# Kernel optimization log

Measured on AMD Instinct MI355X. Metric: run time of the kernel, lower is better.

The kernel has to match this reference:

```python
import jax, jax.numpy as jnp
import numpy as np

HEADS = 8
NQ = 4  # n_qubits


def _apply_rx(state, q, theta):
    # state: (M,2,2,2,2) complex, theta: (M,)
    c = jnp.cos(theta / 2).astype(jnp.complex64)
    s = (-1j * jnp.sin(theta / 2)).astype(jnp.complex64)
    g = jnp.stack([jnp.stack([c, s], -1), jnp.stack([s, c], -1)], -2)  # (M,2,2)
    st = jnp.moveaxis(state, 1 + q, 1)
    st = jnp.einsum('mab,mb...->ma...', g, st)
    return jnp.moveaxis(st, 1, 1 + q)


def _apply_cnot(state, c, t):
    st = jnp.moveaxis(state, [1 + c, 1 + t], [1, 2])  # (M,2(ctrl),2(tgt),...)
    st = jnp.concatenate([st[:, :1], st[:, 1:, ::-1]], axis=1)
    return jnp.moveaxis(st, [1, 2], [1 + c, 1 + t])


def vqc(x, weights):
    # x: (M,4) embedding angles; weights: (L,4) layer RX angles
    M = x.shape[0]
    state = jnp.zeros((M, 2, 2, 2, 2), jnp.complex64).at[:, 0, 0, 0, 0].set(1.0)
    for q in range(NQ):  # AngleEmbedding (RX)
        state = _apply_rx(state, q, x[:, q])
    for l in range(weights.shape[0]):  # BasicEntanglerLayers
        for q in range(NQ):
            state = _apply_rx(state, q, jnp.broadcast_to(weights[l, q], (M,)))
        for q in range(NQ):
            state = _apply_cnot(state, q, (q + 1) % NQ)
    probs = state.real ** 2 + state.imag ** 2  # (M,2,2,2,2)
    z = [jnp.moveaxis(probs, 1 + q, 1)[:, 0].sum((1, 2, 3))
         - jnp.moveaxis(probs, 1 + q, 1)[:, 1].sum((1, 2, 3)) for q in range(NQ)]
    return jnp.stack(z, -1)  # (M,4) PauliZ expvals


def setup_inputs() -> dict:
    key = jax.random.key(0)
    ks = jax.random.split(key, 24)
    B, S, E = 16, 512, 512
    D = E // HEADS
    f = jax.random.normal
    inp = {
        'query': f(ks[0], (B, S, E), jnp.float32),
        'key': f(ks[1], (B, S, E), jnp.float32),
        'value': f(ks[2], (B, S, E), jnp.float32),
        'mask': jnp.ones((B, S, S), jnp.int32),
        'Wq_in': f(ks[3], (NQ, D), jnp.float32) / np.sqrt(D),
        'bq_in': f(ks[4], (NQ,), jnp.float32) / np.sqrt(D),
        'Wk_in': f(ks[5], (NQ, D), jnp.float32) / np.sqrt(D),
        'bk_in': f(ks[6], (NQ,), jnp.float32) / np.sqrt(D),
        'Wv_in': f(ks[7], (NQ, D), jnp.float32) / np.sqrt(D),
        'bv_in': f(ks[8], (NQ,), jnp.float32) / np.sqrt(D),
        'wvq': f(ks[9], (1, NQ), jnp.float32),
        'wvk': f(ks[10], (1, NQ), jnp.float32),
        'wvv': f(ks[11], (1, NQ), jnp.float32),
        'Wq': f(ks[12], (D, NQ), jnp.float32) / np.sqrt(NQ),
        'bq': f(ks[13], (D,), jnp.float32) / np.sqrt(NQ),
        'Wk': f(ks[14], (D, NQ), jnp.float32) / np.sqrt(NQ),
        'bk': f(ks[15], (D,), jnp.float32) / np.sqrt(NQ),
        'Wv': f(ks[16], (D, NQ), jnp.float32) / np.sqrt(NQ),
        'bv': f(ks[17], (D,), jnp.float32) / np.sqrt(NQ),
        'Wo': f(ks[18], (E, 2 * E), jnp.float32) / np.sqrt(2 * E),
        'bo': f(ks[19], (E,), jnp.float32) / np.sqrt(2 * E),
    }
    return inp


def reference(query, key, value, mask, Wq_in, bq_in, Wk_in, bk_in, Wv_in, bv_in,
              wvq, wvk, wvv, Wq, bq, Wk, bk, Wv, bv, Wo, bo):
    B, S, E = query.shape
    H = HEADS
    D = E // H

    def project(x, W_in, b_in, w_vqc, W_out, b_out):
        xh = x.reshape(B, S, H, D)
        xin = jnp.einsum('bshd,qd->bshq', xh, W_in) + b_in  # (B,S,H,NQ)
        xq = vqc(xin.reshape(-1, NQ), w_vqc).reshape(B, S, H, NQ)
        return jnp.einsum('bshq,dq->bshd', xq, W_out) + b_out  # (B,S,H,D)

    Q = project(query, Wq_in, bq_in, wvq, Wq, bq)
    K = project(key, Wk_in, bk_in, wvk, Wk, bk)
    V = project(value, Wv_in, bv_in, wvv, Wv, bv)

    energy = jnp.einsum('bqhd,bkhd->bhqk', Q, K)
    # NOTE: original masked_fill result is discarded (no-op); scale is depth/2
    # due to Python precedence (depth**1/2 == depth/2). Reproduced faithfully.
    attn = jax.nn.softmax(energy / (D / 2.0), axis=-1)
    out = jnp.einsum('bhqv,bvhd->bqhd', attn, V).reshape(B, S, H * D)
    Qf = Q.reshape(B, S, H * D)
    cat = jnp.concatenate([Qf, out], axis=-1)  # (B,S,2E)
    return cat @ Wo.T + bo
```

## Files before the change

kernel.cpp:

```cpp
#include <hip/hip_runtime.h>
#include <hip/hip_bf16.h>

#define B_ 16
#define S_ 512
#define E_ 512
#define H_ 8
#define D_ 64

typedef __hip_bfloat16 bf16;
typedef unsigned short u16;
typedef __attribute__((ext_vector_type(8))) short short8;
typedef __attribute__((ext_vector_type(4))) float floatx4;

__device__ __forceinline__ u16 f2b(float x) {
    bf16 h = __float2bfloat16(x);
    return *reinterpret_cast<u16*>(&h);
}
__device__ __forceinline__ short8 ld8(const u16* p) { return *(const short8*)p; }

template<int CTRL>
__device__ __forceinline__ float qperm(float x) {
    return __builtin_bit_cast(float,
        __builtin_amdgcn_update_dpp(0, __builtin_bit_cast(int, x), CTRL, 0xF, 0xF, true));
}

#define PROJ_ROW_BLOCKS 3072

__global__ __launch_bounds__(256) void proj_kernel(
    const float* __restrict__ q_in, const float* __restrict__ k_in, const float* __restrict__ v_in,
    const float* __restrict__ Wq_in, const float* __restrict__ bq_in,
    const float* __restrict__ Wk_in, const float* __restrict__ bk_in,
    const float* __restrict__ Wv_in, const float* __restrict__ bv_in,
    const float* __restrict__ wvq, const float* __restrict__ wvk, const float* __restrict__ wvv,
    const float* __restrict__ Wq, const float* __restrict__ bq,
    const float* __restrict__ Wk, const float* __restrict__ bk,
    const float* __restrict__ Wv, const float* __restrict__ bv,
    const float* __restrict__ Wo, u16* __restrict__ Wb,
    u16* __restrict__ Qb, u16* __restrict__ Kb, u16* __restrict__ Vb)
{
    if (blockIdx.x >= PROJ_ROW_BLOCKS) {
        const int i = ((blockIdx.x - PROJ_ROW_BLOCKS) * 256 + threadIdx.x) * 8;
        const float4 a = *(const float4*)&Wo[i];
        const float4 b4 = *(const float4*)&Wo[i + 4];
        u16 tmp[8] __attribute__((aligned(16)));
        tmp[0] = f2b(a.x); tmp[1] = f2b(a.y); tmp[2] = f2b(a.z); tmp[3] = f2b(a.w);
        tmp[4] = f2b(b4.x); tmp[5] = f2b(b4.y); tmp[6] = f2b(b4.z); tmp[7] = f2b(b4.w);
        *(short8*)&Wb[i] = *(short8*)tmp;
        return;
    }

    __shared__ __align__(16) float sWin[256];
    __shared__ __align__(16) float sWout[256];
    __shared__ __align__(16) float sbout[64];
    __shared__ float4 sbw;

    const int t = threadIdx.x;
    const int p = blockIdx.x >> 10;

    const float *X, *Win, *bin, *wv, *Wout, *bout;
    u16* dst;
    if (p == 0)      { X = q_in; Win = Wq_in; bin = bq_in; wv = wvq; Wout = Wq; bout = bq; dst = Qb; }
    else if (p == 1) { X = k_in; Win = Wk_in; bin = bk_in; wv = wvk; Wout = Wk; bout = bk; dst = Kb; }
    else             { X = v_in; Win = Wv_in; bin = bv_in; wv = wvv; Wout = Wv; bout = bv; dst = Vb; }

    sWin[t] = Win[t];
    sWout[t] = Wout[t];
    if (t < 64) sbout[t] = bout[t];
    if (t == 0) sbw = make_float4(bin[0] + wv[0], bin[1] + wv[1],
                                  bin[2] + wv[2], bin[3] + wv[3]);
    __syncthreads();

    const int j = t & 3;
    const int m = (blockIdx.x & 1023) * 64 + (t >> 2);
    const int d0 = j * 16;

    const float* xp = X + (size_t)m * 64 + d0;
    float4 xv[4];
#pragma unroll
    for (int i = 0; i < 4; ++i) xv[i] = *(const float4*)(xp + i * 4);

    float part[4] = {0.f, 0.f, 0.f, 0.f};
#pragma unroll
    for (int i = 0; i < 4; ++i) {
#pragma unroll
        for (int q = 0; q < 4; ++q) {
            const float4 w4 = *(const float4*)&sWin[q * 64 + d0 + i * 4];
            part[q] = fmaf(xv[i].x, w4.x, fmaf(xv[i].y, w4.y,
                      fmaf(xv[i].z, w4.z, fmaf(xv[i].w, w4.w, part[q]))));
        }
    }
#pragma unroll
    for (int q = 0; q < 4; ++q) {
        part[q] += qperm<0xB1>(part[q]);
        part[q] += qperm<0x4E>(part[q]);
    }

    const float4 bw = sbw;
    const float c0 = __cosf(part[0] + bw.x);
    const float c1 = __cosf(part[1] + bw.y);
    const float c2 = __cosf(part[2] + bw.z);
    const float c3 = __cosf(part[3] + bw.w);
    const float tt = c2 * c3;
    const float z1 = c0 * c1;
    const float z0 = c1 * tt;
    const float z2 = z1 * c2;
    const float z3 = z1 * tt;

    const int b = m >> 12, s = (m >> 3) & 511, h = m & 7;
    u16* op = dst + ((size_t)(b * 4096 + h * 512 + s)) * 64 + d0;

    u16 tmp[16] __attribute__((aligned(16)));
#pragma unroll
    for (int d = 0; d < 16; ++d) {
        const float4 wo = *(const float4*)&sWout[(d0 + d) * 4];
        const float o = fmaf(z0, wo.x, fmaf(z1, wo.y,
                        fmaf(z2, wo.z, fmaf(z3, wo.w, sbout[d0 + d]))));
        tmp[d] = f2b(o);
    }
    *(short8*)op = *(short8*)tmp;
    *(short8*)(op + 8) = *(short8*)(tmp + 8);
}

__global__ __launch_bounds__(256) void attn_kernel(
    const u16* __restrict__ Qb, const u16* __restrict__ Kb, const u16* __restrict__ Vb,
    u16* __restrict__ Ob)
{
    __shared__ __align__(16) u16 Ks[64][72];
    __shared__ __align__(16) u16 Vt[64][72];
    __shared__ __align__(16) u16 Ps[4][32][72];

    const int t = threadIdx.x, lane = t & 63, w = t >> 6;
    const int bh = blockIdx.x >> 2;
    const int q0 = (blockIdx.x & 3) * 128;
    const int b = bh >> 3, h = bh & 7;

    const u16* Qp = Qb + (size_t)bh * (S_ * D_) + (size_t)q0 * D_;
    const u16* Kp = Kb + (size_t)bh * (S_ * D_);
    const u16* Vp = Vb + (size_t)bh * (S_ * D_);

    const int nl = lane & 15;
    const int kg = (lane >> 4) * 8;

    short8 qa[2][2];
#pragma unroll
    for (int mt = 0; mt < 2; ++mt) {
        qa[mt][0] = ld8(&Qp[(w * 32 + mt * 16 + nl) * 64 + kg]);
        qa[mt][1] = ld8(&Qp[(w * 32 + mt * 16 + nl) * 64 + kg + 32]);
    }

    floatx4 of[2][4];
    float l_run[2][4];
#pragma unroll
    for (int mt = 0; mt < 2; ++mt)
#pragma unroll
        for (int r = 0; r < 4; ++r) { l_run[mt][r] = 0.f; }
#pragma unroll
    for (int mt = 0; mt < 2; ++mt)
#pragma unroll
        for (int nt = 0; nt < 4; ++nt) of[mt][nt] = 0.f;

    const int rK = t & 63, cK = (t >> 6) * 8;
    const int vr0 = (t & 31) * 2, vc = (t >> 5) * 8;

    short8 kA = ld8(&Kp[rK * 64 + cK]);
    short8 kB = ld8(&Kp[rK * 64 + cK + 32]);
    short8 vA = ld8(&Vp[vr0 * 64 + vc]);
    short8 vB = ld8(&Vp[(vr0 + 1) * 64 + vc]);

    for (int ch = 0; ch < 8; ++ch) {
        __syncthreads();
        *(short8*)&Ks[rK][cK] = kA;
        *(short8*)&Ks[rK][cK + 32] = kB;
#pragma unroll
        for (int jj = 0; jj < 8; ++jj) {
            const unsigned pack = (u16)((short*)&vA)[jj] |
                                  ((unsigned)(u16)((short*)&vB)[jj] << 16);
            *(unsigned*)&Vt[vc + jj][vr0] = pack;
        }
        if (ch < 7) {
            const int nb = (ch + 1) * 64;
            kA = ld8(&Kp[(nb + rK) * 64 + cK]);
            kB = ld8(&Kp[(nb + rK) * 64 + cK + 32]);
            vA = ld8(&Vp[(nb + vr0) * 64 + vc]);
            vB = ld8(&Vp[(nb + vr0 + 1) * 64 + vc]);
        }
        __syncthreads();

        floatx4 sf[2][4];
#pragma unroll
        for (int mt = 0; mt < 2; ++mt)
#pragma unroll
            for (int nt = 0; nt < 4; ++nt) sf[mt][nt] = 0.f;
#pragma unroll
        for (int nt = 0; nt < 4; ++nt) {
            const short8 kf0 = ld8(&Ks[nt * 16 + nl][kg]);
            const short8 kf1 = ld8(&Ks[nt * 16 + nl][kg + 32]);
#pragma unroll
            for (int mt = 0; mt < 2; ++mt) {
                sf[mt][nt] = __builtin_amdgcn_mfma_f32_16x16x32_bf16(qa[mt][0], kf0, sf[mt][nt], 0, 0, 0);
                sf[mt][nt] = __builtin_amdgcn_mfma_f32_16x16x32_bf16(qa[mt][1], kf1, sf[mt][nt], 0, 0, 0);
            }
        }

        const int prow = (lane >> 4) * 4;
#pragma unroll
        for (int mt = 0; mt < 2; ++mt)
#pragma unroll
            for (int nt = 0; nt < 4; ++nt) {
#pragma unroll
                for (int r = 0; r < 4; ++r) {
                    const float pv = __expf(sf[mt][nt][r] * 0.03125f);
                    l_run[mt][r] += pv;
                    Ps[w][mt * 16 + prow + r][nt * 16 + nl] = f2b(pv);
                }
            }

        short8 pa[2][2];
#pragma unroll
        for (int mt = 0; mt < 2; ++mt) {
            pa[mt][0] = ld8(&Ps[w][mt * 16 + nl][kg]);
            pa[mt][1] = ld8(&Ps[w][mt * 16 + nl][kg + 32]);
        }
#pragma unroll
        for (int nt = 0; nt < 4; ++nt) {
            const short8 vf0 = ld8(&Vt[nt * 16 + nl][kg]);
            const short8 vf1 = ld8(&Vt[nt * 16 + nl][kg + 32]);
#pragma unroll
            for (int mt = 0; mt < 2; ++mt) {
                of[mt][nt] = __builtin_amdgcn_mfma_f32_16x16x32_bf16(pa[mt][0], vf0, of[mt][nt], 0, 0, 0);
                of[mt][nt] = __builtin_amdgcn_mfma_f32_16x16x32_bf16(pa[mt][1], vf1, of[mt][nt], 0, 0, 0);
            }
        }
    }

#pragma unroll
    for (int mt = 0; mt < 2; ++mt) {
        float inv[4];
#pragma unroll
        for (int r = 0; r < 4; ++r) {
            float sum = l_run[mt][r];
#pragma unroll
            for (int off = 1; off < 16; off <<= 1) sum += __shfl_xor(sum, off, 64);
            inv[r] = 1.0f / sum;
        }
        const int srow = q0 + w * 32 + mt * 16 + (lane >> 4) * 4;
#pragma unroll
        for (int r = 0; r < 4; ++r) {
            const size_t base = ((size_t)(b * S_ + srow + r)) * E_ + h * 64 + nl;
#pragma unroll
            for (int nt = 0; nt < 4; ++nt)
                Ob[base + nt * 16] = f2b(of[mt][nt][r] * inv[r]);
        }
    }
}

__global__ __launch_bounds__(256) void out_kernel(
    const u16* __restrict__ Qb, const u16* __restrict__ Ob,
    const u16* __restrict__ Wb, const float* __restrict__ bo,
    float* __restrict__ out)
{
    __shared__ __align__(16) u16 As[64][72];
    __shared__ __align__(16) u16 Bs[128][72];

    const int t = threadIdx.x, lane = t & 63, w = t >> 6;
    const int e0 = (blockIdx.x & 3) * 128;
    const int n0 = (blockIdx.x >> 2) * 64;
    const int wr = (w >> 1) * 32, wc = (w & 1) * 64;
    const int nl = lane & 15, kg = (lane >> 4) * 8;

    const int rA = t & 63, cA = (t >> 6) * 8;
    const int rB = t & 127, cB0 = (t >> 7) * 8;
    const u16* wrow = &Wb[(size_t)(e0 + rB) * 1024];

    floatx4 acc[2][4];
#pragma unroll
    for (int i = 0; i < 2; ++i)
#pragma unroll
        for (int jq = 0; jq < 4; ++jq) acc[i][jq] = 0.f;

    auto a_src = [&](int j0, int r, int c) -> const u16* {
        const int n = n0 + r;
        return (j0 < 512)
            ? &Qb[(((size_t)(n >> 9) * 8 + (j0 >> 6)) * 512 + (n & 511)) * 64 + c]
            : &Ob[(size_t)n * 512 + (j0 - 512) + c];
    };

    short8 aA = ld8(a_src(0, rA, cA));
    short8 aB = ld8(a_src(0, rA, cA + 32));
    short8 b0 = ld8(wrow + cB0);
    short8 b1 = ld8(wrow + cB0 + 16);
    short8 b2 = ld8(wrow + cB0 + 32);
    short8 b3 = ld8(wrow + cB0 + 48);

    for (int j0 = 0; j0 < 1024; j0 += 64) {
        __syncthreads();
        *(short8*)&As[rA][cA] = aA;
        *(short8*)&As[rA][cA + 32] = aB;
        *(short8*)&Bs[rB][cB0] = b0;
        *(short8*)&Bs[rB][cB0 + 16] = b1;
        *(short8*)&Bs[rB][cB0 + 32] = b2;
        *(short8*)&Bs[rB][cB0 + 48] = b3;
        if (j0 < 960) {
            const int jn = j0 + 64;
            aA = ld8(a_src(jn, rA, cA));
            aB = ld8(a_src(jn, rA, cA + 32));
            b0 = ld8(wrow + jn + cB0);
            b1 = ld8(wrow + jn + cB0 + 16);
            b2 = ld8(wrow + jn + cB0 + 32);
            b3 = ld8(wrow + jn + cB0 + 48);
        }
        __syncthreads();

        short8 af[2][2], bfr[4][2];
#pragma unroll
        for (int mt = 0; mt < 2; ++mt) {
            af[mt][0] = ld8(&As[wr + mt * 16 + nl][kg]);
            af[mt][1] = ld8(&As[wr + mt * 16 + nl][kg + 32]);
        }
#pragma unroll
        for (int nt = 0; nt < 4; ++nt) {
            bfr[nt][0] = ld8(&Bs[wc + nt * 16 + nl][kg]);
            bfr[nt][1] = ld8(&Bs[wc + nt * 16 + nl][kg + 32]);
        }
#pragma unroll
        for (int mt = 0; mt < 2; ++mt)
#pragma unroll
            for (int nt = 0; nt < 4; ++nt) {
                acc[mt][nt] = __builtin_amdgcn_mfma_f32_16x16x32_bf16(af[mt][0], bfr[nt][0], acc[mt][nt], 0, 0, 0);
                acc[mt][nt] = __builtin_amdgcn_mfma_f32_16x16x32_bf16(af[mt][1], bfr[nt][1], acc[mt][nt], 0, 0, 0);
            }
    }

    const int prow = (lane >> 4) * 4;
#pragma unroll
    for (int mt = 0; mt < 2; ++mt)
#pragma unroll
        for (int r = 0; r < 4; ++r) {
            const int n = n0 + wr + mt * 16 + prow + r;
#pragma unroll
            for (int nt = 0; nt < 4; ++nt) {
                const int e = e0 + wc + nt * 16 + nl;
                out[(size_t)n * 512 + e] = acc[mt][nt][r] + bo[e];
            }
        }
}

extern "C" void kernel_launch(void* const* d_in, const int* in_sizes, int n_in,
                              void* d_out, int out_size, void* d_ws, size_t ws_size,
                              hipStream_t stream)
{
    const float* q_in  = (const float*)d_in[0];
    const float* k_in  = (const float*)d_in[1];
    const float* v_in  = (const float*)d_in[2];
    const float* Wq_in = (const float*)d_in[4];
    const float* bq_in = (const float*)d_in[5];
    const float* Wk_in = (const float*)d_in[6];
    const float* bk_in = (const float*)d_in[7];
    const float* Wv_in = (const float*)d_in[8];
    const float* bv_in = (const float*)d_in[9];
    const float* wvq   = (const float*)d_in[10];
    const float* wvk   = (const float*)d_in[11];
    const float* wvv   = (const float*)d_in[12];
    const float* Wq    = (const float*)d_in[13];
    const float* bq    = (const float*)d_in[14];
    const float* Wk    = (const float*)d_in[15];
    const float* bk    = (const float*)d_in[16];
    const float* Wv    = (const float*)d_in[17];
    const float* bv    = (const float*)d_in[18];
    const float* Wo    = (const float*)d_in[19];
    const float* bo    = (const float*)d_in[20];

    u16* ws = (u16*)d_ws;
    u16* Qb = ws;
    u16* Kb = ws + (size_t)(1 << 22);
    u16* Vb = ws + (size_t)(2 << 22);
    u16* Ob = ws + (size_t)3 * (1 << 22);
    u16* Wb = ws + (size_t)4 * (1 << 22);

    proj_kernel<<<PROJ_ROW_BLOCKS + 256, 256, 0, stream>>>(q_in, k_in, v_in,
        Wq_in, bq_in, Wk_in, bk_in, Wv_in, bv_in,
        wvq, wvk, wvv, Wq, bq, Wk, bk, Wv, bv,
        Wo, Wb, Qb, Kb, Vb);
    attn_kernel<<<512, 256, 0, stream>>>(Qb, Kb, Vb, Ob);
    out_kernel<<<512, 256, 0, stream>>>(Qb, Ob, Wb, bo, (float*)d_out);
}
```

Baseline: 186.0 us.

## Load MFMA operand fragments directly from global memory, dropping LDS staging for K and GEMM

```diff
diff --git a/kernel.cpp b/kernel.cpp
--- a/kernel.cpp
+++ b/kernel.cpp
@@ -121,11 +121,10 @@
     *(short8*)(op + 8) = *(short8*)(tmp + 8);
 }
 
-__global__ __launch_bounds__(256) void attn_kernel(
+__global__ __launch_bounds__(256, 2) void attn_kernel(
     const u16* __restrict__ Qb, const u16* __restrict__ Kb, const u16* __restrict__ Vb,
     u16* __restrict__ Ob)
 {
-    __shared__ __align__(16) u16 Ks[64][72];
     __shared__ __align__(16) u16 Vt[64][72];
     __shared__ __align__(16) u16 Ps[4][32][72];
 
@@ -153,24 +152,26 @@
 #pragma unroll
     for (int mt = 0; mt < 2; ++mt)
 #pragma unroll
-        for (int r = 0; r < 4; ++r) { l_run[mt][r] = 0.f; }
+        for (int r = 0; r < 4; ++r) l_run[mt][r] = 0.f;
 #pragma unroll
     for (int mt = 0; mt < 2; ++mt)
 #pragma unroll
         for (int nt = 0; nt < 4; ++nt) of[mt][nt] = 0.f;
 
-    const int rK = t & 63, cK = (t >> 6) * 8;
     const int vr0 = (t & 31) * 2, vc = (t >> 5) * 8;
 
-    short8 kA = ld8(&Kp[rK * 64 + cK]);
-    short8 kB = ld8(&Kp[rK * 64 + cK + 32]);
+    short8 kf[2][4][2];
+#pragma unroll
+    for (int nt = 0; nt < 4; ++nt) {
+        kf[0][nt][0] = ld8(&Kp[(nt * 16 + nl) * 64 + kg]);
+        kf[0][nt][1] = ld8(&Kp[(nt * 16 + nl) * 64 + kg + 32]);
+    }
     short8 vA = ld8(&Vp[vr0 * 64 + vc]);
     short8 vB = ld8(&Vp[(vr0 + 1) * 64 + vc]);
 
     for (int ch = 0; ch < 8; ++ch) {
+        const int cur = ch & 1, nxt = cur ^ 1;
         __syncthreads();
-        *(short8*)&Ks[rK][cK] = kA;
-        *(short8*)&Ks[rK][cK + 32] = kB;
 #pragma unroll
         for (int jj = 0; jj < 8; ++jj) {
             const unsigned pack = (u16)((short*)&vA)[jj] |
@@ -179,8 +180,11 @@
         }
         if (ch < 7) {
             const int nb = (ch + 1) * 64;
-            kA = ld8(&Kp[(nb + rK) * 64 + cK]);
-            kB = ld8(&Kp[(nb + rK) * 64 + cK + 32]);
+#pragma unroll
+            for (int nt = 0; nt < 4; ++nt) {
+                kf[nxt][nt][0] = ld8(&Kp[(nb + nt * 16 + nl) * 64 + kg]);
+                kf[nxt][nt][1] = ld8(&Kp[(nb + nt * 16 + nl) * 64 + kg + 32]);
+            }
             vA = ld8(&Vp[(nb + vr0) * 64 + vc]);
             vB = ld8(&Vp[(nb + vr0 + 1) * 64 + vc]);
         }
@@ -193,12 +197,10 @@
             for (int nt = 0; nt < 4; ++nt) sf[mt][nt] = 0.f;
 #pragma unroll
         for (int nt = 0; nt < 4; ++nt) {
-            const short8 kf0 = ld8(&Ks[nt * 16 + nl][kg]);
-            const short8 kf1 = ld8(&Ks[nt * 16 + nl][kg + 32]);
 #pragma unroll
             for (int mt = 0; mt < 2; ++mt) {
-                sf[mt][nt] = __builtin_amdgcn_mfma_f32_16x16x32_bf16(qa[mt][0], kf0, sf[mt][nt], 0, 0, 0);
-                sf[mt][nt] = __builtin_amdgcn_mfma_f32_16x16x32_bf16(qa[mt][1], kf1, sf[mt][nt], 0, 0, 0);
+                sf[mt][nt] = __builtin_amdgcn_mfma_f32_16x16x32_bf16(qa[mt][0], kf[cur][nt][0], sf[mt][nt], 0, 0, 0);
+                sf[mt][nt] = __builtin_amdgcn_mfma_f32_16x16x32_bf16(qa[mt][1], kf[cur][nt][1], sf[mt][nt], 0, 0, 0);
             }
         }
 
@@ -254,80 +256,69 @@
     }
 }
 
-__global__ __launch_bounds__(256) void out_kernel(
+__global__ __launch_bounds__(256, 2) void out_kernel(
     const u16* __restrict__ Qb, const u16* __restrict__ Ob,
     const u16* __restrict__ Wb, const float* __restrict__ bo,
     float* __restrict__ out)
 {
-    __shared__ __align__(16) u16 As[64][72];
-    __shared__ __align__(16) u16 Bs[128][72];
-
-    const int t = threadIdx.x, lane = t & 63, w = t >> 6;
+    const int lane = threadIdx.x & 63, w = threadIdx.x >> 6;
     const int e0 = (blockIdx.x & 3) * 128;
     const int n0 = (blockIdx.x >> 2) * 64;
     const int wr = (w >> 1) * 32, wc = (w & 1) * 64;
     const int nl = lane & 15, kg = (lane >> 4) * 8;
 
-    const int rA = t & 63, cA = (t >> 6) * 8;
-    const int rB = t & 127, cB0 = (t >> 7) * 8;
-    const u16* wrow = &Wb[(size_t)(e0 + rB) * 1024];
-
     floatx4 acc[2][4];
 #pragma unroll
     for (int i = 0; i < 2; ++i)
 #pragma unroll
         for (int jq = 0; jq < 4; ++jq) acc[i][jq] = 0.f;
 
-    auto a_src = [&](int j0, int r, int c) -> const u16* {
-        const int n = n0 + r;
+    const int an[2] = { n0 + wr + nl, n0 + wr + 16 + nl };
+    const u16* wrow[4];
+#pragma unroll
+    for (int nt = 0; nt < 4; ++nt)
+        wrow[nt] = &Wb[(size_t)(e0 + wc + nt * 16 + nl) * 1024];
+
+    auto a_src = [&](int j0, int n, int c) -> const u16* {
         return (j0 < 512)
             ? &Qb[(((size_t)(n >> 9) * 8 + (j0 >> 6)) * 512 + (n & 511)) * 64 + c]
             : &Ob[(size_t)n * 512 + (j0 - 512) + c];
     };
 
-    short8 aA = ld8(a_src(0, rA, cA));
-    short8 aB = ld8(a_src(0, rA, cA + 32));
-    short8 b0 = ld8(wrow + cB0);
-    short8 b1 = ld8(wrow + cB0 + 16);
-    short8 b2 = ld8(wrow + cB0 + 32);
-    short8 b3 = ld8(wrow + cB0 + 48);
-
-    for (int j0 = 0; j0 < 1024; j0 += 64) {
-        __syncthreads();
-        *(short8*)&As[rA][cA] = aA;
-        *(short8*)&As[rA][cA + 32] = aB;
-        *(short8*)&Bs[rB][cB0] = b0;
-        *(short8*)&Bs[rB][cB0 + 16] = b1;
-        *(short8*)&Bs[rB][cB0 + 32] = b2;
-        *(short8*)&Bs[rB][cB0 + 48] = b3;
-        if (j0 < 960) {
-            const int jn = j0 + 64;
-            aA = ld8(a_src(jn, rA, cA));
-            aB = ld8(a_src(jn, rA, cA + 32));
-            b0 = ld8(wrow + jn + cB0);
-            b1 = ld8(wrow + jn + cB0 + 16);
-            b2 = ld8(wrow + jn + cB0 + 32);
-            b3 = ld8(wrow + jn + cB0 + 48);
-        }
-        __syncthreads();
-
-        short8 af[2][2], bfr[4][2];
-#pragma unroll
-        for (int mt = 0; mt < 2; ++mt) {
-            af[mt][0] = ld8(&As[wr + mt * 16 + nl][kg]);
-            af[mt][1] = ld8(&As[wr + mt * 16 + nl][kg + 32]);
-        }
-#pragma unroll
-        for (int nt = 0; nt < 4; ++nt) {
-            bfr[nt][0] = ld8(&Bs[wc + nt * 16 + nl][kg]);
-            bfr[nt][1] = ld8(&Bs[wc + nt * 16 + nl][kg + 32]);
+    short8 af[2][2][2], bf[2][4][2];
+#pragma unroll
+    for (int mt = 0; mt < 2; ++mt) {
+        af[0][mt][0] = ld8(a_src(0, an[mt], kg));
+        af[0][mt][1] = ld8(a_src(0, an[mt], kg + 32));
+    }
+#pragma unroll
+    for (int nt = 0; nt < 4; ++nt) {
+        bf[0][nt][0] = ld8(wrow[nt] + kg);
+        bf[0][nt][1] = ld8(wrow[nt] + kg + 32);
+    }
+
+#pragma unroll
+    for (int sl = 0; sl < 16; ++sl) {
+        const int cur = sl & 1, nxt = cur ^ 1;
+        if (sl < 15) {
+            const int jn = (sl + 1) * 64;
+#pragma unroll
+            for (int mt = 0; mt < 2; ++mt) {
+                af[nxt][mt][0] = ld8(a_src(jn, an[mt], kg));
+                af[nxt][mt][1] = ld8(a_src(jn, an[mt], kg + 32));
+            }
+#pragma unroll
+            for (int nt = 0; nt < 4; ++nt) {
+                bf[nxt][nt][0] = ld8(wrow[nt] + jn + kg);
+                bf[nxt][nt][1] = ld8(wrow[nt] + jn + kg + 32);
+            }
         }
 #pragma unroll
         for (int mt = 0; mt < 2; ++mt)
 #pragma unroll
             for (int nt = 0; nt < 4; ++nt) {
-                acc[mt][nt] = __builtin_amdgcn_mfma_f32_16x16x32_bf16(af[mt][0], bfr[nt][0], acc[mt][nt], 0, 0, 0);
-                acc[mt][nt] = __builtin_amdgcn_mfma_f32_16x16x32_bf16(af[mt][1], bfr[nt][1], acc[mt][nt], 0, 0, 0);
+                acc[mt][nt] = __builtin_amdgcn_mfma_f32_16x16x32_bf16(af[cur][mt][0], bf[cur][nt][0], acc[mt][nt], 0, 0, 0);
+                acc[mt][nt] = __builtin_amdgcn_mfma_f32_16x16x32_bf16(af[cur][mt][1], bf[cur][nt][1], acc[mt][nt], 0, 0, 0);
             }
     }
 
```

New measurement: 208.5 us. 12.1% more time.
